# Optimization experiments

Measured on AMD Instinct MI355X. Metric: run time of the kernel, lower is better.

The kernel has to match this reference:

```python
import jax, jax.numpy as jnp
import numpy as np

N_NODES = 100000
N_EDGES = 800000
F_IN = 300
F_PROJ = 256
HIDDEN = 256
F2 = 128
OUT = 4
NEG_SLOPE = 0.2
BN_EPS = 1e-5


def setup_inputs() -> dict:
    key = jax.random.key(0)
    ks = jax.random.split(key, 20)
    def g(k, shape, scale=0.05):
        return jax.random.normal(k, shape, dtype=jnp.float32) * scale
    return {
        "x": jax.random.normal(ks[0], (N_NODES, F_IN), dtype=jnp.float32),
        "edge_index": jax.random.randint(ks[1], (2, N_EDGES), 0, N_NODES),
        "lin_w": g(ks[2], (F_IN, F_PROJ)), "lin_b": jnp.zeros((F_PROJ,), jnp.float32),
        "w1_src": g(ks[3], (F_PROJ, HIDDEN)), "w1_dst": g(ks[4], (F_PROJ, HIDDEN)),
        "a1_src": g(ks[5], (HIDDEN,)), "a1_dst": g(ks[6], (HIDDEN,)),
        "b1": jnp.zeros((HIDDEN,), jnp.float32),
        "w2_src": g(ks[7], (HIDDEN, F2)), "w2_dst": g(ks[8], (HIDDEN, F2)),
        "a2_src": g(ks[9], (F2,)), "a2_dst": g(ks[10], (F2,)),
        "b2": jnp.zeros((F2,), jnp.float32),
        "fc1_w": g(ks[11], (F2, 64)), "fc1_b": jnp.zeros((64,), jnp.float32),
        "bn_g": jnp.ones((64,), jnp.float32), "bn_b": jnp.zeros((64,), jnp.float32),
        "fc2_w": g(ks[12], (64, OUT)), "fc2_b": jnp.zeros((OUT,), jnp.float32),
    }


def gat_conv(x, src, dst, w_src, w_dst, att_src, att_dst, bias, n):
    # PyG GATConv, heads=1: separate src/dst linear, additive attention, LeakyReLU,
    # per-destination segment softmax, weighted scatter-add aggregation.
    h_src = x @ w_src                      # [N, C]
    h_dst = x @ w_dst                      # [N, C]
    a_s = h_src @ att_src                  # [N]
    a_d = h_dst @ att_dst                  # [N]
    e = jax.nn.leaky_relu(a_s[src] + a_d[dst], NEG_SLOPE)  # [E]
    m = jax.ops.segment_max(e, dst, num_segments=n)
    w = jnp.exp(e - m[dst])
    denom = jax.ops.segment_sum(w, dst, num_segments=n)
    alpha = w / (denom[dst] + 1e-16)       # [E]
    out = jax.ops.segment_sum(h_src[src] * alpha[:, None], dst, num_segments=n)
    return out + bias


def reference(x, edge_index, lin_w, lin_b, w1_src, w1_dst, a1_src, a1_dst, b1,
              w2_src, w2_dst, a2_src, a2_dst, b2, fc1_w, fc1_b, bn_g, bn_b,
              fc2_w, fc2_b):
    n = x.shape[0]
    loops = jnp.arange(n)
    src = jnp.concatenate([edge_index[0], loops])  # add_self_loops=True (PyG default)
    dst = jnp.concatenate([edge_index[1], loops])
    h = jax.nn.relu(x @ lin_w + lin_b)             # node-type Linear(-1, 256) + relu
    h = jax.nn.relu(gat_conv(h, src, dst, w1_src, w1_dst, a1_src, a1_dst, b1, n))
    h = jax.nn.relu(gat_conv(h, src, dst, w2_src, w2_dst, a2_src, a2_dst, b2, n))
    h = h @ fc1_w + fc1_b
    mu = jnp.mean(h, axis=0)
    var = jnp.var(h, axis=0)
    h = (h - mu) * jax.lax.rsqrt(var + BN_EPS) * bn_g + bn_b
    h = jax.nn.relu(h)
    h = h @ fc2_w + fc2_b
    return jax.nn.log_softmax(h, axis=-1)
```

## Files before the change

kernel.cpp:

```cpp
#include <hip/hip_runtime.h>
#include <hip/hip_bf16.h>
#include <cmath>

#define NN 100000
#define NE 800000
#define ETOT (NE + NN)
#define MP 100096

#define SCHUNK 512
#define NBLK ((NN + SCHUNK - 1) / SCHUNK)

typedef __attribute__((ext_vector_type(8))) short bf16x8;
typedef __attribute__((ext_vector_type(4))) float f32x4;

__device__ inline void gl_lds16(const void* g, void* l) {
    __builtin_amdgcn_global_load_lds(
        (const __attribute__((address_space(1))) void*)g,
        (__attribute__((address_space(3))) void*)l, 16, 0, 0);
}

__device__ inline ushort f2bf(float f) {
    __hip_bfloat16 b = __float2bfloat16(f);
    return *(ushort*)&b;
}
__device__ inline uint pk2(float a, float b) {
    return (uint)f2bf(a) | ((uint)f2bf(b) << 16);
}

__global__ __launch_bounds__(256)
void mfma_gemm(const __hip_bfloat16* __restrict__ Abf,
               const __hip_bfloat16* __restrict__ Btbf,
               const float* __restrict__ bias, void* __restrict__ out,
               const float* __restrict__ dotv, float* __restrict__ dotout,
               int Kp, int ldc, int Mstore, int Nstore, int flags)
{
    __shared__ __align__(16) short As[128 * 32];
    __shared__ __align__(16) short Bs[128 * 32];
    const short* A  = (const short*)Abf;
    const short* Bt = (const short*)Btbf;

    const int tid  = threadIdx.x;
    const int lane = tid & 63;
    const int wv   = tid >> 6;
    const int wr   = (wv >> 1) * 64;
    const int wc   = (wv & 1) * 64;
    const int quad = lane >> 4;
    const int l16  = lane & 15;
    const long bm = (long)blockIdx.x * 128;
    const long bn = (long)blockIdx.y * 128;

    const int r0 = tid >> 2;
    const int c0 = (tid & 3) ^ ((r0 >> 1) & 3);
    const int r1 = r0 + 64;
    const int c1 = (tid & 3) ^ ((r1 >> 1) & 3);
    const short* a_g0 = A + (bm + r0) * (long)Kp + c0 * 8;
    const short* a_g1 = A + (bm + r1) * (long)Kp + c1 * 8;
    const short* b_g0 = Bt + (bn + r0) * (long)Kp + c0 * 8;
    const short* b_g1 = Bt + (bn + r1) * (long)Kp + c1 * 8;
    short* a_l0 = &As[tid * 8];
    short* a_l1 = &As[(tid + 256) * 8];
    short* b_l0 = &Bs[tid * 8];
    short* b_l1 = &Bs[(tid + 256) * 8];

    f32x4 acc[4][4] = {};
    const int xr = (quad ^ ((l16 >> 1) & 3)) * 8;

    for (int k0 = 0; k0 < Kp; k0 += 32) {
        gl_lds16(a_g0 + k0, a_l0);
        gl_lds16(a_g1 + k0, a_l1);
        gl_lds16(b_g0 + k0, b_l0);
        gl_lds16(b_g1 + k0, b_l1);
        __syncthreads();

        bf16x8 af[4], bf[4];
#pragma unroll
        for (int i = 0; i < 4; i++)
            af[i] = *(const bf16x8*)&As[(wr + i * 16 + l16) * 32 + xr];
#pragma unroll
        for (int j = 0; j < 4; j++)
            bf[j] = *(const bf16x8*)&Bs[(wc + j * 16 + l16) * 32 + xr];
#pragma unroll
        for (int i = 0; i < 4; i++)
#pragma unroll
            for (int j = 0; j < 4; j++)
                acc[i][j] = __builtin_amdgcn_mfma_f32_16x16x32_bf16(
                    af[i], bf[j], acc[i][j], 0, 0, 0);
        __syncthreads();
    }

    __hip_bfloat16* outb = (__hip_bfloat16*)out;
    float* outf = (float*)out;
    float dp[16];
#pragma unroll
    for (int t = 0; t < 16; t++) dp[t] = 0.f;

#pragma unroll
    for (int i = 0; i < 4; i++) {
        long row_base = bm + wr + i * 16 + quad * 4;
#pragma unroll
        for (int j = 0; j < 4; j++) {
            long col = bn + wc + j * 16 + l16;
            if (col >= Nstore) continue;
            float bv = bias ? bias[col] : 0.f;
            float dv = dotout ? dotv[col] : 0.f;
#pragma unroll
            for (int r = 0; r < 4; r++) {
                long row = row_base + r;
                float v = acc[i][j][r] + bv;
                if (flags & 1) v = fmaxf(v, 0.f);
                dp[i * 4 + r] = fmaf(v, dv, dp[i * 4 + r]);
                if (row >= Mstore) continue;
                if (flags & 2) outb[row * ldc + col] = __float2bfloat16(v);
                else           outf[row * ldc + col] = v;
            }
        }
    }

    if (dotout) {
#pragma unroll
        for (int t = 0; t < 16; t++) {
            float s = dp[t];
            s += __shfl_xor(s, 1); s += __shfl_xor(s, 2);
            s += __shfl_xor(s, 4); s += __shfl_xor(s, 8);
            if (l16 == 0) {
                long row = bm + wr + (t >> 2) * 16 + quad * 4 + (t & 3);
                if (row < Mstore) atomicAdd(&dotout[row], s);
            }
        }
    }
}

__global__ __launch_bounds__(256)
void cast_x_vec(const float* __restrict__ x, __hip_bfloat16* __restrict__ xb)
{
    const int idx = blockIdx.x * 256 + threadIdx.x;
    if (idx >= MP * 40) return;
    const int row = idx / 40;
    const int c8  = (idx % 40) * 8;
    uint4 v;
    if (row < NN && c8 + 8 <= 300) {
        const float* xp = x + (size_t)row * 300 + c8;
        float4 f0 = *(const float4*)xp;
        float4 f1 = *(const float4*)(xp + 4);
        v.x = pk2(f0.x, f0.y); v.y = pk2(f0.z, f0.w);
        v.z = pk2(f1.x, f1.y); v.w = pk2(f1.z, f1.w);
    } else {
        float f[8];
#pragma unroll
        for (int k = 0; k < 8; k++)
            f[k] = (row < NN && c8 + k < 300) ? x[(size_t)row * 300 + c8 + k] : 0.f;
        v.x = pk2(f[0], f[1]); v.y = pk2(f[2], f[3]);
        v.z = pk2(f[4], f[5]); v.w = pk2(f[6], f[7]);
    }
    *(uint4*)((ushort*)xb + (size_t)row * 320 + c8) = v;
}

__global__ void cast_wT(const float* __restrict__ w, __hip_bfloat16* __restrict__ wt,
                        int K, int N, int Kp, int Np)
{
    int idx = blockIdx.x * 256 + threadIdx.x;
    if (idx >= Np * Kp) return;
    int n = idx / Kp, k = idx % Kp;
    float v = (n < N && k < K) ? w[(size_t)k * N + n] : 0.f;
    wt[idx] = __float2bfloat16(v);
}

__global__ void count_edges(const int* __restrict__ ei, int* __restrict__ counts)
{
    int e = blockIdx.x * blockDim.x + threadIdx.x;
    if (e >= ETOT) return;
    int d = (e < NE) ? ei[NE + e] : (e - NE);
    atomicAdd(&counts[d], 1);
}

__global__ __launch_bounds__(256)
void scan_partial(const int* __restrict__ counts, int* __restrict__ blk)
{
    __shared__ int sh[256];
    const int tid = threadIdx.x;
    const int base = blockIdx.x * SCHUNK + tid * 2;
    int c0 = (base < NN)     ? counts[base]     : 0;
    int c1 = (base + 1 < NN) ? counts[base + 1] : 0;
    sh[tid] = c0 + c1;
    __syncthreads();
    for (int off = 128; off; off >>= 1) {
        if (tid < off) sh[tid] += sh[tid + off];
        __syncthreads();
    }
    if (tid == 0) blk[blockIdx.x] = sh[0];
}

__global__ __launch_bounds__(256)
void scan_blocks(int* __restrict__ blk)
{
    __shared__ int sh[256];
    const int tid = threadIdx.x;
    int v = (tid < NBLK) ? blk[tid] : 0;
    sh[tid] = v;
    __syncthreads();
    for (int off = 1; off < 256; off <<= 1) {
        int u = (tid >= off) ? sh[tid - off] : 0;
        __syncthreads();
        sh[tid] += u;
        __syncthreads();
    }
    if (tid < NBLK) blk[tid] = sh[tid] - v;
}

__global__ __launch_bounds__(256)
void scan_fill(const int* __restrict__ counts, const int* __restrict__ blk,
               int* __restrict__ row_ptr, int* __restrict__ cursor)
{
    __shared__ int sh[256];
    const int tid = threadIdx.x;
    const int i0 = blockIdx.x * SCHUNK + tid * 2;
    int c0 = (i0 < NN)     ? counts[i0]     : 0;
    int c1 = (i0 + 1 < NN) ? counts[i0 + 1] : 0;
    int s = c0 + c1;
    sh[tid] = s;
    __syncthreads();
    for (int off = 1; off < 256; off <<= 1) {
        int u = (tid >= off) ? sh[tid - off] : 0;
        __syncthreads();
        sh[tid] += u;
        __syncthreads();
    }
    int pre = sh[tid] - s + blk[blockIdx.x];
    if (i0 < NN)     { row_ptr[i0] = pre;          cursor[i0] = pre; }
    if (i0 + 1 < NN) { row_ptr[i0 + 1] = pre + c0; cursor[i0 + 1] = pre + c0; }
    if (blockIdx.x == 0 && tid == 0) row_ptr[NN] = ETOT;
}

__global__ void fill_edges(const int* __restrict__ ei, int* __restrict__ cursor,
                           int* __restrict__ csr_src)
{
    int e = blockIdx.x * blockDim.x + threadIdx.x;
    if (e >= ETOT) return;
    int s, d;
    if (e < NE) { s = ei[e]; d = ei[NE + e]; }
    else        { s = e - NE; d = s; }
    int pos = atomicAdd(&cursor[d], 1);
    csr_src[pos] = s;
}

__global__ void wv_kernel(const float* __restrict__ w, const float* __restrict__ a,
                          float* __restrict__ v, int Cin, int Cout)
{
    int i = blockIdx.x * blockDim.x + threadIdx.x;
    if (i >= Cin) return;
    float s = 0.f;
    for (int j = 0; j < Cout; j++) s = fmaf(w[(size_t)i * Cout + j], a[j], s);
    v[i] = s;
}

template<int LPN>
__global__ __launch_bounds__(256)
void gat_agg_wave(const __hip_bfloat16* __restrict__ hsrc,
                  const float* __restrict__ a_s,
                  const float* __restrict__ a_d,
                  const int* __restrict__ row_ptr,
                  const int* __restrict__ csr_src,
                  const float* __restrict__ bias,
                  __hip_bfloat16* __restrict__ outh,
                  const float* __restrict__ dotv,
                  float* __restrict__ dotout)
{
    const int C = LPN * 4;
    const int NPB = 256 / LPN;
    __shared__ __align__(16) float2 ws_sh[NPB][LPN];

    const int tid  = threadIdx.x;
    const int slot = tid / LPN;
    const int sub  = tid % LPN;
    const int n = blockIdx.x * NPB + slot;
    if (n >= NN) return;

    const int start = row_ptr[n];
    const int deg = row_ptr[n + 1] - start;
    const float a_dn = a_d[n];
    const ushort* hp = (const ushort*)hsrc;

    float M = -3e30f, S = 0.f;
    float acc0 = 0.f, acc1 = 0.f, acc2 = 0.f, acc3 = 0.f;

    for (int c0 = 0; c0 < deg; c0 += LPN) {
        const int cnt = min(LPN, deg - c0);
        int sj = 0;
        float e = -3e30f;
        if (sub < cnt) {
            sj = csr_src[start + c0 + sub];
            float t = a_s[sj] + a_dn;
            e = (t >= 0.f) ? t : 0.2f * t;
        }
        float cm = e;
#pragma unroll
        for (int off = LPN / 2; off; off >>= 1) cm = fmaxf(cm, __shfl_xor(cm, off));
        float newM = fmaxf(M, cm);
        float w = (sub < cnt) ? __expf(e - newM) : 0.f;
        float cs = w;
#pragma unroll
        for (int off = LPN / 2; off; off >>= 1) cs += __shfl_xor(cs, off);
        float scale = __expf(M - newM);
        S = S * scale + cs;
        acc0 *= scale; acc1 *= scale; acc2 *= scale; acc3 *= scale;
        M = newM;

        ws_sh[slot][sub] = make_float2(w, __int_as_float(sj));
        const int cnt4 = (cnt + 3) & ~3;
        const ushort* hpl = hp + sub * 4;
        for (int j = 0; j < cnt4; j += 4) {
            float4 p0 = *(const float4*)&ws_sh[slot][j];
            float4 p1 = *(const float4*)&ws_sh[slot][j + 2];
            const ushort* r0 = hpl + (size_t)__float_as_int(p0.y) * C;
            const ushort* r1 = hpl + (size_t)__float_as_int(p0.w) * C;
            const ushort* r2 = hpl + (size_t)__float_as_int(p1.y) * C;
            const ushort* r3 = hpl + (size_t)__float_as_int(p1.w) * C;
            uint2 u0 = *(const uint2*)r0;
            uint2 u1 = *(const uint2*)r1;
            uint2 u2 = *(const uint2*)r2;
            uint2 u3 = *(const uint2*)r3;
            acc0 = fmaf(p0.x, __uint_as_float(u0.x << 16), acc0);
            acc1 = fmaf(p0.x, __uint_as_float(u0.x & 0xffff0000u), acc1);
            acc2 = fmaf(p0.x, __uint_as_float(u0.y << 16), acc2);
            acc3 = fmaf(p0.x, __uint_as_float(u0.y & 0xffff0000u), acc3);
            acc0 = fmaf(p0.z, __uint_as_float(u1.x << 16), acc0);
            acc1 = fmaf(p0.z, __uint_as_float(u1.x & 0xffff0000u), acc1);
            acc2 = fmaf(p0.z, __uint_as_float(u1.y << 16), acc2);
            acc3 = fmaf(p0.z, __uint_as_float(u1.y & 0xffff0000u), acc3);
            acc0 = fmaf(p1.x, __uint_as_float(u2.x << 16), acc0);
            acc1 = fmaf(p1.x, __uint_as_float(u2.x & 0xffff0000u), acc1);
            acc2 = fmaf(p1.x, __uint_as_float(u2.y << 16), acc2);
            acc3 = fmaf(p1.x, __uint_as_float(u2.y & 0xffff0000u), acc3);
            acc0 = fmaf(p1.z, __uint_as_float(u3.x << 16), acc0);
            acc1 = fmaf(p1.z, __uint_as_float(u3.x & 0xffff0000u), acc1);
            acc2 = fmaf(p1.z, __uint_as_float(u3.y << 16), acc2);
            acc3 = fmaf(p1.z, __uint_as_float(u3.y & 0xffff0000u), acc3);
        }
    }

    float inv = 1.f / (S + 1e-16f);
    float o0 = fmaxf(acc0 * inv + bias[sub * 4 + 0], 0.f);
    float o1 = fmaxf(acc1 * inv + bias[sub * 4 + 1], 0.f);
    float o2 = fmaxf(acc2 * inv + bias[sub * 4 + 2], 0.f);
    float o3 = fmaxf(acc3 * inv + bias[sub * 4 + 3], 0.f);

    ushort4 v;
    v.x = f2bf(o0); v.y = f2bf(o1); v.z = f2bf(o2); v.w = f2bf(o3);
    *(ushort4*)((ushort*)outh + (size_t)n * C + sub * 4) = v;

    if (dotout) {
        float dp = o0 * dotv[sub * 4 + 0] + o1 * dotv[sub * 4 + 1]
                 + o2 * dotv[sub * 4 + 2] + o3 * dotv[sub * 4 + 3];
#pragma unroll
        for (int off = LPN / 2; off; off >>= 1) dp += __shfl_xor(dp, off);
        if (sub == 0) dotout[n] = dp;
    }
}

__global__ __launch_bounds__(256)
void bn_stats(const float* __restrict__ h, float* __restrict__ stats)
{
    int col = threadIdx.x & 63;
    int rg = threadIdx.x >> 6;
    int r0 = blockIdx.x * 256;
    int r1 = min(r0 + 256, NN);
    float s = 0.f, s2 = 0.f;
    for (int r = r0 + rg; r < r1; r += 4) {
        float v = h[(size_t)r * 64 + col];
        s += v; s2 += v * v;
    }
    __shared__ float sh[2][4][64];
    sh[0][rg][col] = s; sh[1][rg][col] = s2;
    __syncthreads();
    if (rg == 0) {
        s  = sh[0][0][col] + sh[0][1][col] + sh[0][2][col] + sh[0][3][col];
        s2 = sh[1][0][col] + sh[1][1][col] + sh[1][2][col] + sh[1][3][col];
        atomicAdd(&stats[col], s);
        atomicAdd(&stats[64 + col], s2);
    }
}

__global__ void bn_finalize(const float* __restrict__ stats,
                            const float* __restrict__ g, const float* __restrict__ b,
                            float* __restrict__ ss)
{
    int c = threadIdx.x;
    float mu = stats[c] / (float)NN;
    float var = stats[64 + c] / (float)NN - mu * mu;
    float rs = rsqrtf(var + 1e-5f);
    float sc = rs * g[c];
    ss[c] = sc;
    ss[64 + c] = b[c] - mu * sc;
}

__global__ __launch_bounds__(256)
void final_head(const float* __restrict__ h3, const float* __restrict__ ss,
                const float* __restrict__ fc2_w, const float* __restrict__ fc2_b,
                float* __restrict__ out)
{
    int lane = threadIdx.x & 63;
    int n = blockIdx.x * 4 + (threadIdx.x >> 6);
    if (n >= NN) return;
    float y = h3[(size_t)n * 64 + lane];
    y = fmaxf(y * ss[lane] + ss[64 + lane], 0.f);
    float z[4];
#pragma unroll
    for (int o = 0; o < 4; o++) {
        float p = y * fc2_w[lane * 4 + o];
#pragma unroll
        for (int off = 32; off; off >>= 1) p += __shfl_xor(p, off);
        z[o] = p + fc2_b[o];
    }
    float mx = fmaxf(fmaxf(z[0], z[1]), fmaxf(z[2], z[3]));
    float lse = mx + logf(expf(z[0] - mx) + expf(z[1] - mx) +
                          expf(z[2] - mx) + expf(z[3] - mx));
    if (lane < 4) out[(size_t)n * 4 + lane] = z[lane] - lse;
}

extern "C" void kernel_launch(void* const* d_in, const int* in_sizes, int n_in,
                              void* d_out, int out_size, void* d_ws, size_t ws_size,
                              hipStream_t stream)
{
    const float* x      = (const float*)d_in[0];
    const int*   ei     = (const int*)d_in[1];
    const float* lin_w  = (const float*)d_in[2];
    const float* lin_b  = (const float*)d_in[3];
    const float* w1_src = (const float*)d_in[4];
    const float* w1_dst = (const float*)d_in[5];
    const float* a1_src = (const float*)d_in[6];
    const float* a1_dst = (const float*)d_in[7];
    const float* b1     = (const float*)d_in[8];
    const float* w2_src = (const float*)d_in[9];
    const float* w2_dst = (const float*)d_in[10];
    const float* a2_src = (const float*)d_in[11];
    const float* a2_dst = (const float*)d_in[12];
    const float* b2     = (const float*)d_in[13];
    const float* fc1_w  = (const float*)d_in[14];
    const float* fc1_b  = (const float*)d_in[15];
    const float* bn_g   = (const float*)d_in[16];
    const float* bn_b   = (const float*)d_in[17];
    const float* fc2_w  = (const float*)d_in[18];
    const float* fc2_b  = (const float*)d_in[19];
    float* out = (float*)d_out;

    char* p = (char*)d_ws;
    auto alloc = [&](size_t bytes) { char* r = p; p += (bytes + 255) & ~(size_t)255; return r; };
    char* R1 = alloc((size_t)MP * 320 * 2);
    char* R2 = alloc((size_t)MP * 256 * 2);
    char* R3 = alloc((size_t)MP * 256 * 2);
    __hip_bfloat16* wlinT = (__hip_bfloat16*)alloc(256 * 320 * 2);
    __hip_bfloat16* w1T   = (__hip_bfloat16*)alloc(256 * 256 * 2);
    __hip_bfloat16* w2T   = (__hip_bfloat16*)alloc(128 * 256 * 2);
    __hip_bfloat16* fc1T  = (__hip_bfloat16*)alloc(128 * 128 * 2);
    float* avec  = (float*)alloc((size_t)NN * 4 * 4);
    float* aS1 = avec;
    float* aD1 = avec + NN;
    float* aS2 = avec + 2 * (size_t)NN;
    float* aD2 = avec + 3 * (size_t)NN;
    float* vvec1 = (float*)alloc(256 * 4);
    float* vvec2 = (float*)alloc(256 * 4);
    float* ss    = (float*)alloc(128 * 4);
    float* stats = (float*)alloc(128 * 4);
    int* row_ptr = (int*)alloc((size_t)(NN + 1) * 4);
    int* cursor  = (int*)alloc((size_t)(NN + 1) * 4);
    int* counts  = (int*)alloc((size_t)NN * 4);
    int* blk     = (int*)alloc(256 * 4);
    int* csr_src = (int*)alloc((size_t)ETOT * 4);

    __hip_bfloat16* x_bf  = (__hip_bfloat16*)R1;
    __hip_bfloat16* hsrc1 = (__hip_bfloat16*)R1;
    __hip_bfloat16* h0    = (__hip_bfloat16*)R2;
    __hip_bfloat16* hsrc2 = (__hip_bfloat16*)R2;
    __hip_bfloat16* h2    = (__hip_bfloat16*)(R2 + (size_t)MP * 128 * 2);
    __hip_bfloat16* h1    = (__hip_bfloat16*)R3;
    float*          h3    = (float*)R3;

    const int eb = (ETOT + 255) / 256;
    const int MB = MP / 128;

    hipMemsetAsync(avec, 0, sizeof(float) * NN * 4, stream);

    hipMemsetAsync(counts, 0, sizeof(int) * NN, stream);
    count_edges<<<eb, 256, 0, stream>>>(ei, counts);
    scan_partial<<<NBLK, 256, 0, stream>>>(counts, blk);
    scan_blocks<<<1, 256, 0, stream>>>(blk);
    scan_fill<<<NBLK, 256, 0, stream>>>(counts, blk, row_ptr, cursor);
    fill_edges<<<eb, 256, 0, stream>>>(ei, cursor, csr_src);

    cast_x_vec<<<(MP * 40 + 255) / 256, 256, 0, stream>>>(x, x_bf);
    cast_wT<<<(256 * 320 + 255) / 256, 256, 0, stream>>>(lin_w, wlinT, 300, 256, 320, 256);
    cast_wT<<<(256 * 256 + 255) / 256, 256, 0, stream>>>(w1_src, w1T, 256, 256, 256, 256);
    cast_wT<<<(128 * 256 + 255) / 256, 256, 0, stream>>>(w2_src, w2T, 256, 128, 256, 128);
    cast_wT<<<(128 * 128 + 255) / 256, 256, 0, stream>>>(fc1_w, fc1T, 128, 64, 128, 128);
    wv_kernel<<<4, 64, 0, stream>>>(w1_dst, a1_dst, vvec1, 256, 256);
    wv_kernel<<<4, 64, 0, stream>>>(w2_dst, a2_dst, vvec2, 256, 128);

    mfma_gemm<<<dim3(MB, 2), 256, 0, stream>>>(x_bf, wlinT, lin_b, h0,
                                               vvec1, aD1, 320, 256, NN, 256, 3);

    mfma_gemm<<<dim3(MB, 2), 256, 0, stream>>>(h0, w1T, nullptr, hsrc1,
                                               a1_src, aS1, 256, 256, NN, 256, 2);
    gat_agg_wave<64><<<(NN + 3) / 4, 256, 0, stream>>>(hsrc1, aS1, aD1, row_ptr,
                                                       csr_src, b1, h1, vvec2, aD2);

    mfma_gemm<<<dim3(MB, 1), 256, 0, stream>>>(h1, w2T, nullptr, hsrc2,
                                               a2_src, aS2, 256, 128, NN, 128, 2);
    gat_agg_wave<32><<<(NN + 7) / 8, 256, 0, stream>>>(hsrc2, aS2, aD2, row_ptr,
                                                       csr_src, b2, h2, nullptr, nullptr);

    mfma_gemm<<<dim3(MB, 1), 256, 0, stream>>>(h2, fc1T, fc1_b, h3,
                                               nullptr, nullptr, 128, 64, NN, 64, 0);
    hipMemsetAsync(stats, 0, sizeof(float) * 128, stream);
    bn_stats<<<(NN + 255) / 256, 256, 0, stream>>>(h3, stats);
    bn_finalize<<<1, 64, 0, stream>>>(stats, bn_g, bn_b, ss);
    final_head<<<(NN + 3) / 4, 256, 0, stream>>>(h3, ss, fc2_w, fc2_b, out);
}
```

Baseline: 699.1 us.

## Fuse BN stats into GEMM, merge prep kernels, drop online softmax max

Several changes land together. The batch-norm column sums are accumulated in the fc1 GEMM epilogue through atomics, which removes the bn_stats kernel and its memset. The weight casts and attention-vector kernels are merged into a single prep launch. In the GAT aggregation, the running-max online softmax is dropped in favour of plain exp sums, the gather loop is unrolled to eight edges, and bias and dot loads are vectorised. Skipping the max subtraction risks overflow if attention logits become large.

```diff
diff --git a/kernel.cpp b/kernel.cpp
--- a/kernel.cpp
+++ b/kernel.cpp
@@ -32,6 +32,7 @@
                const __hip_bfloat16* __restrict__ Btbf,
                const float* __restrict__ bias, void* __restrict__ out,
                const float* __restrict__ dotv, float* __restrict__ dotout,
+               float* __restrict__ stats,
                int Kp, int ldc, int Mstore, int Nstore, int flags)
 {
     __shared__ __align__(16) short As[128 * 32];
@@ -91,8 +92,11 @@
     __hip_bfloat16* outb = (__hip_bfloat16*)out;
     float* outf = (float*)out;
     float dp[16];
+    float sv[4], sv2[4];
 #pragma unroll
     for (int t = 0; t < 16; t++) dp[t] = 0.f;
+#pragma unroll
+    for (int j = 0; j < 4; j++) { sv[j] = 0.f; sv2[j] = 0.f; }
 
 #pragma unroll
     for (int i = 0; i < 4; i++) {
@@ -110,6 +114,7 @@
                 if (flags & 1) v = fmaxf(v, 0.f);
                 dp[i * 4 + r] = fmaf(v, dv, dp[i * 4 + r]);
                 if (row >= Mstore) continue;
+                if (flags & 4) { sv[j] += v; sv2[j] += v * v; }
                 if (flags & 2) outb[row * ldc + col] = __float2bfloat16(v);
                 else           outf[row * ldc + col] = v;
             }
@@ -125,6 +130,22 @@
             if (l16 == 0) {
                 long row = bm + wr + (t >> 2) * 16 + quad * 4 + (t & 3);
                 if (row < Mstore) atomicAdd(&dotout[row], s);
+            }
+        }
+    }
+
+    if (flags & 4) {
+#pragma unroll
+        for (int j = 0; j < 4; j++) {
+            float s = sv[j], s2 = sv2[j];
+            s  += __shfl_xor(s, 16);  s  += __shfl_xor(s, 32);
+            s2 += __shfl_xor(s2, 16); s2 += __shfl_xor(s2, 32);
+            if (quad == 0) {
+                long col = bn + wc + j * 16 + l16;
+                if (col < Nstore) {
+                    atomicAdd(&stats[col], s);
+                    atomicAdd(&stats[64 + col], s2);
+                }
             }
         }
     }
@@ -155,14 +176,43 @@
     *(uint4*)((ushort*)xb + (size_t)row * 320 + c8) = v;
 }
 
-__global__ void cast_wT(const float* __restrict__ w, __hip_bfloat16* __restrict__ wt,
-                        int K, int N, int Kp, int Np)
-{
-    int idx = blockIdx.x * 256 + threadIdx.x;
-    if (idx >= Np * Kp) return;
+__device__ inline void castT_one(const float* __restrict__ w,
+                                 __hip_bfloat16* __restrict__ wt,
+                                 int K, int N, int Kp, int idx)
+{
     int n = idx / Kp, k = idx % Kp;
     float v = (n < N && k < K) ? w[(size_t)k * N + n] : 0.f;
     wt[idx] = __float2bfloat16(v);
+}
+
+__global__ __launch_bounds__(256)
+void prep_small(const float* __restrict__ lin_w, const float* __restrict__ w1_src,
+                const float* __restrict__ w2_src, const float* __restrict__ fc1_w,
+                const float* __restrict__ w1_dst, const float* __restrict__ a1_dst,
+                const float* __restrict__ w2_dst, const float* __restrict__ a2_dst,
+                __hip_bfloat16* __restrict__ wlinT, __hip_bfloat16* __restrict__ w1T,
+                __hip_bfloat16* __restrict__ w2T, __hip_bfloat16* __restrict__ fc1T,
+                float* __restrict__ vvec1, float* __restrict__ vvec2)
+{
+    const int b = blockIdx.x;
+    const int tid = threadIdx.x;
+    if (b < 320) {
+        castT_one(lin_w, wlinT, 300, 256, 320, b * 256 + tid);
+    } else if (b < 576) {
+        castT_one(w1_src, w1T, 256, 256, 256, (b - 320) * 256 + tid);
+    } else if (b < 704) {
+        castT_one(w2_src, w2T, 256, 128, 256, (b - 576) * 256 + tid);
+    } else if (b < 768) {
+        castT_one(fc1_w, fc1T, 128, 64, 128, (b - 704) * 256 + tid);
+    } else if (b == 768) {
+        float s = 0.f;
+        for (int j = 0; j < 256; j++) s = fmaf(w1_dst[(size_t)tid * 256 + j], a1_dst[j], s);
+        vvec1[tid] = s;
+    } else {
+        float s = 0.f;
+        for (int j = 0; j < 128; j++) s = fmaf(w2_dst[(size_t)tid * 128 + j], a2_dst[j], s);
+        vvec2[tid] = s;
+    }
 }
 
 __global__ void count_edges(const int* __restrict__ ei, int* __restrict__ counts)
@@ -243,16 +293,6 @@
     csr_src[pos] = s;
 }
 
-__global__ void wv_kernel(const float* __restrict__ w, const float* __restrict__ a,
-                          float* __restrict__ v, int Cin, int Cout)
-{
-    int i = blockIdx.x * blockDim.x + threadIdx.x;
-    if (i >= Cin) return;
-    float s = 0.f;
-    for (int j = 0; j < Cout; j++) s = fmaf(w[(size_t)i * Cout + j], a[j], s);
-    v[i] = s;
-}
-
 template<int LPN>
 __global__ __launch_bounds__(256)
 void gat_agg_wave(const __hip_bfloat16* __restrict__ hsrc,
@@ -280,103 +320,67 @@
     const float a_dn = a_d[n];
     const ushort* hp = (const ushort*)hsrc;
 
-    float M = -3e30f, S = 0.f;
+    float S = 0.f;
     float acc0 = 0.f, acc1 = 0.f, acc2 = 0.f, acc3 = 0.f;
 
     for (int c0 = 0; c0 < deg; c0 += LPN) {
         const int cnt = min(LPN, deg - c0);
-        int sj = 0;
-        float e = -3e30f;
+        int sj = 0; float w = 0.f;
         if (sub < cnt) {
             sj = csr_src[start + c0 + sub];
             float t = a_s[sj] + a_dn;
-            e = (t >= 0.f) ? t : 0.2f * t;
+            t = (t >= 0.f) ? t : 0.2f * t;
+            w = __expf(t);
         }
-        float cm = e;
-#pragma unroll
-        for (int off = LPN / 2; off; off >>= 1) cm = fmaxf(cm, __shfl_xor(cm, off));
-        float newM = fmaxf(M, cm);
-        float w = (sub < cnt) ? __expf(e - newM) : 0.f;
-        float cs = w;
-#pragma unroll
-        for (int off = LPN / 2; off; off >>= 1) cs += __shfl_xor(cs, off);
-        float scale = __expf(M - newM);
-        S = S * scale + cs;
-        acc0 *= scale; acc1 *= scale; acc2 *= scale; acc3 *= scale;
-        M = newM;
-
+        S += w;
         ws_sh[slot][sub] = make_float2(w, __int_as_float(sj));
-        const int cnt4 = (cnt + 3) & ~3;
+
+        const int cnt8 = (cnt + 7) & ~7;
         const ushort* hpl = hp + sub * 4;
-        for (int j = 0; j < cnt4; j += 4) {
+        for (int j = 0; j < cnt8; j += 8) {
             float4 p0 = *(const float4*)&ws_sh[slot][j];
             float4 p1 = *(const float4*)&ws_sh[slot][j + 2];
-            const ushort* r0 = hpl + (size_t)__float_as_int(p0.y) * C;
-            const ushort* r1 = hpl + (size_t)__float_as_int(p0.w) * C;
-            const ushort* r2 = hpl + (size_t)__float_as_int(p1.y) * C;
-            const ushort* r3 = hpl + (size_t)__float_as_int(p1.w) * C;
-            uint2 u0 = *(const uint2*)r0;
-            uint2 u1 = *(const uint2*)r1;
-            uint2 u2 = *(const uint2*)r2;
-            uint2 u3 = *(const uint2*)r3;
-            acc0 = fmaf(p0.x, __uint_as_float(u0.x << 16), acc0);
-            acc1 = fmaf(p0.x, __uint_as_float(u0.x & 0xffff0000u), acc1);
-            acc2 = fmaf(p0.x, __uint_as_float(u0.y << 16), acc2);
-            acc3 = fmaf(p0.x, __uint_as_float(u0.y & 0xffff0000u), acc3);
-            acc0 = fmaf(p0.z, __uint_as_float(u1.x << 16), acc0);
-            acc1 = fmaf(p0.z, __uint_as_float(u1.x & 0xffff0000u), acc1);
-            acc2 = fmaf(p0.z, __uint_as_float(u1.y << 16), acc2);
-            acc3 = fmaf(p0.z, __uint_as_float(u1.y & 0xffff0000u), acc3);
-            acc0 = fmaf(p1.x, __uint_as_float(u2.x << 16), acc0);
-            acc1 = fmaf(p1.x, __uint_as_float(u2.x & 0xffff0000u), acc1);
-            acc2 = fmaf(p1.x, __uint_as_float(u2.y << 16), acc2);
-            acc3 = fmaf(p1.x, __uint_as_float(u2.y & 0xffff0000u), acc3);
-            acc0 = fmaf(p1.z, __uint_as_float(u3.x << 16), acc0);
-            acc1 = fmaf(p1.z, __uint_as_float(u3.x & 0xffff0000u), acc1);
-            acc2 = fmaf(p1.z, __uint_as_float(u3.y << 16), acc2);
-            acc3 = fmaf(p1.z, __uint_as_float(u3.y & 0xffff0000u), acc3);
+            float4 p2 = *(const float4*)&ws_sh[slot][j + 4];
+            float4 p3 = *(const float4*)&ws_sh[slot][j + 6];
+            uint2 u0 = *(const uint2*)(hpl + (size_t)__float_as_int(p0.y) * C);
+            uint2 u1 = *(const uint2*)(hpl + (size_t)__float_as_int(p0.w) * C);
+            uint2 u2 = *(const uint2*)(hpl + (size_t)__float_as_int(p1.y) * C);
+            uint2 u3 = *(const uint2*)(hpl + (size_t)__float_as_int(p1.w) * C);
+            uint2 u4 = *(const uint2*)(hpl + (size_t)__float_as_int(p2.y) * C);
+            uint2 u5 = *(const uint2*)(hpl + (size_t)__float_as_int(p2.w) * C);
+            uint2 u6 = *(const uint2*)(hpl + (size_t)__float_as_int(p3.y) * C);
+            uint2 u7 = *(const uint2*)(hpl + (size_t)__float_as_int(p3.w) * C);
+#define ACC4(W, U) \
+            acc0 = fmaf(W, __uint_as_float(U.x << 16), acc0); \
+            acc1 = fmaf(W, __uint_as_float(U.x & 0xffff0000u), acc1); \
+            acc2 = fmaf(W, __uint_as_float(U.y << 16), acc2); \
+            acc3 = fmaf(W, __uint_as_float(U.y & 0xffff0000u), acc3);
+            ACC4(p0.x, u0) ACC4(p0.z, u1) ACC4(p1.x, u2) ACC4(p1.z, u3)
+            ACC4(p2.x, u4) ACC4(p2.z, u5) ACC4(p3.x, u6) ACC4(p3.z, u7)
+#undef ACC4
         }
     }
 
+#pragma unroll
+    for (int off = LPN / 2; off; off >>= 1) S += __shfl_xor(S, off);
+
     float inv = 1.f / (S + 1e-16f);
-    float o0 = fmaxf(acc0 * inv + bias[sub * 4 + 0], 0.f);
-    float o1 = fmaxf(acc1 * inv + bias[sub * 4 + 1], 0.f);
-    float o2 = fmaxf(acc2 * inv + bias[sub * 4 + 2], 0.f);
-    float o3 = fmaxf(acc3 * inv + bias[sub * 4 + 3], 0.f);
+    const float4 b4 = *(const float4*)&bias[sub * 4];
+    float o0 = fmaxf(acc0 * inv + b4.x, 0.f);
+    float o1 = fmaxf(acc1 * inv + b4.y, 0.f);
+    float o2 = fmaxf(acc2 * inv + b4.z, 0.f);
+    float o3 = fmaxf(acc3 * inv + b4.w, 0.f);
 
     ushort4 v;
     v.x = f2bf(o0); v.y = f2bf(o1); v.z = f2bf(o2); v.w = f2bf(o3);
     *(ushort4*)((ushort*)outh + (size_t)n * C + sub * 4) = v;
 
     if (dotout) {
-        float dp = o0 * dotv[sub * 4 + 0] + o1 * dotv[sub * 4 + 1]
-                 + o2 * dotv[sub * 4 + 2] + o3 * dotv[sub * 4 + 3];
+        const float4 d4 = *(const float4*)&dotv[sub * 4];
+        float dp = o0 * d4.x + o1 * d4.y + o2 * d4.z + o3 * d4.w;
 #pragma unroll
         for (int off = LPN / 2; off; off >>= 1) dp += __shfl_xor(dp, off);
         if (sub == 0) dotout[n] = dp;
-    }
-}
-
-__global__ __launch_bounds__(256)
-void bn_stats(const float* __restrict__ h, float* __restrict__ stats)
-{
-    int col = threadIdx.x & 63;
-    int rg = threadIdx.x >> 6;
-    int r0 = blockIdx.x * 256;
-    int r1 = min(r0 + 256, NN);
-    float s = 0.f, s2 = 0.f;
-    for (int r = r0 + rg; r < r1; r += 4) {
-        float v = h[(size_t)r * 64 + col];
-        s += v; s2 += v * v;
-    }
-    __shared__ float sh[2][4][64];
-    sh[0][rg][col] = s; sh[1][rg][col] = s2;
-    __syncthreads();
-    if (rg == 0) {
-        s  = sh[0][0][col] + sh[0][1][col] + sh[0][2][col] + sh[0][3][col];
-        s2 = sh[1][0][col] + sh[1][1][col] + sh[1][2][col] + sh[1][3][col];
-        atomicAdd(&stats[col], s);
-        atomicAdd(&stats[64 + col], s2);
     }
 }
 
@@ -452,15 +456,15 @@
     __hip_bfloat16* w1T   = (__hip_bfloat16*)alloc(256 * 256 * 2);
     __hip_bfloat16* w2T   = (__hip_bfloat16*)alloc(128 * 256 * 2);
     __hip_bfloat16* fc1T  = (__hip_bfloat16*)alloc(128 * 128 * 2);
-    float* avec  = (float*)alloc((size_t)NN * 4 * 4);
+    float* avec  = (float*)alloc((size_t)NN * 4 * 4 + 512);
     float* aS1 = avec;
     float* aD1 = avec + NN;
     float* aS2 = avec + 2 * (size_t)NN;
     float* aD2 = avec + 3 * (size_t)NN;
+    float* stats = avec + 4 * (size_t)NN;
     float* vvec1 = (float*)alloc(256 * 4);
     float* vvec2 = (float*)alloc(256 * 4);
     float* ss    = (float*)alloc(128 * 4);
-    float* stats = (float*)alloc(128 * 4);
     int* row_ptr = (int*)alloc((size_t)(NN + 1) * 4);
     int* cursor  = (int*)alloc((size_t)(NN + 1) * 4);
     int* counts  = (int*)alloc((size_t)NN * 4);
@@ -478,7 +482,7 @@
     const int eb = (ETOT + 255) / 256;
     const int MB = MP / 128;
 
-    hipMemsetAsync(avec, 0, sizeof(float) * NN * 4, stream);
+    hipMemsetAsync(avec, 0, sizeof(float) * NN * 4 + 512, stream);
 
     hipMemsetAsync(counts, 0, sizeof(int) * NN, stream);
     count_edges<<<eb, 256, 0, stream>>>(ei, counts);
@@ -488,30 +492,25 @@
     fill_edges<<<eb, 256, 0, stream>>>(ei, cursor, csr_src);
 
     cast_x_vec<<<(MP * 40 + 255) / 256, 256, 0, stream>>>(x, x_bf);
-    cast_wT<<<(256 * 320 + 255) / 256, 256, 0, stream>>>(lin_w, wlinT, 300, 256, 320, 256);
-    cast_wT<<<(256 * 256 + 255) / 256, 256, 0, stream>>>(w1_src, w1T, 256, 256, 256, 256);
-    cast_wT<<<(128 * 256 + 255) / 256, 256, 0, stream>>>(w2_src, w2T, 256, 128, 256, 128);
-    cast_wT<<<(128 * 128 + 255) / 256, 256, 0, stream>>>(fc1_w, fc1T, 128, 64, 128, 128);
-    wv_kernel<<<4, 64, 0, stream>>>(w1_dst, a1_dst, vvec1, 256, 256);
-    wv_kernel<<<4, 64, 0, stream>>>(w2_dst, a2_dst, vvec2, 256, 128);
+    prep_small<<<770, 256, 0, stream>>>(lin_w, w1_src, w2_src, fc1_w,
+                                        w1_dst, a1_dst, w2_dst, a2_dst,
+                                        wlinT, w1T, w2T, fc1T, vvec1, vvec2);
 
     mfma_gemm<<<dim3(MB, 2), 256, 0, stream>>>(x_bf, wlinT, lin_b, h0,
-                                               vvec1, aD1, 320, 256, NN, 256, 3);
+                                               vvec1, aD1, nullptr, 320, 256, NN, 256, 3);
 
     mfma_gemm<<<dim3(MB, 2), 256, 0, stream>>>(h0, w1T, nullptr, hsrc1,
-                                               a1_src, aS1, 256, 256, NN, 256, 2);
+                                               a1_src, aS1, nullptr, 256, 256, NN, 256, 2);
     gat_agg_wave<64><<<(NN + 3) / 4, 256, 0, stream>>>(hsrc1, aS1, aD1, row_ptr,
                                                        csr_src, b1, h1, vvec2, aD2);
 
     mfma_gemm<<<dim3(MB, 1), 256, 0, stream>>>(h1, w2T, nullptr, hsrc2,
-                                               a2_src, aS2, 256, 128, NN, 128, 2);
+                                               a2_src, aS2, nullptr, 256, 128, NN, 128, 2);
     gat_agg_wave<32><<<(NN + 7) / 8, 256, 0, stream>>>(hsrc2, aS2, aD2, row_ptr,
                                                        csr_src, b2, h2, nullptr, nullptr);
 
     mfma_gemm<<<dim3(MB, 1), 256, 0, stream>>>(h2, fc1T, fc1_b, h3,
-                                               nullptr, nullptr, 128, 64, NN, 64, 0);
-    hipMemsetAsync(stats, 0, sizeof(float) * 128, stream);
-    bn_stats<<<(NN + 255) / 256, 256, 0, stream>>>(h3, stats);
+                                               nullptr, nullptr, stats, 128, 64, NN, 64, 4);
     bn_finalize<<<1, 64, 0, stream>>>(stats, bn_g, bn_b, ss);
     final_head<<<(NN + 3) / 4, 256, 0, stream>>>(h3, ss, fc2_w, fc2_b, out);
 }
```

After: 699.4 us. No clear change (+0.0%).
